# Kernel tuning notes

Measured on AMD Instinct MI355X. Metric: run time of the kernel, lower is better.

The kernel has to match this reference:

```python
import jax, jax.numpy as jnp
import numpy as np

N, E = 50000, 640000
D_IN, D_OUT, N_BASES = 128, 128, 8


def setup_inputs() -> dict:
    key = jax.random.key(0)
    k1, k2, k3, k4, k5, k6 = jax.random.split(key, 6)
    x = jax.random.normal(k1, (N, D_IN), dtype=jnp.float32)
    edge_index = jax.random.randint(k2, (2, E), 0, N, dtype=jnp.int64)
    # basis-decomposed relation weights (num_relations=1)
    bases = jax.random.normal(k3, (N_BASES, D_IN, D_OUT), dtype=jnp.float32) * 0.05
    comp = jax.random.normal(k4, (1, N_BASES), dtype=jnp.float32)
    root = jax.random.normal(k5, (D_IN, D_OUT), dtype=jnp.float32) * 0.05
    bias = jax.random.normal(k6, (D_OUT,), dtype=jnp.float32) * 0.01
    return {"x": x, "edge_index": edge_index, "bases": bases,
            "comp": comp, "root": root, "bias": bias}


def reference(x, edge_index, bases, comp, root, bias):
    # W[rel=0] = sum_b comp[0,b] * bases[b]  -> [D_IN, D_OUT]
    W = jnp.einsum('b,bio->io', comp[0], bases)
    src = edge_index[0]  # message sources (x_j)
    dst = edge_index[1]  # aggregation targets
    # gather -> scatter-add (aggr='add'), then relation-specific transform
    agg = jax.ops.segment_sum(x[src], dst, num_segments=x.shape[0])  # [N, D_IN]
    out = agg @ W + x @ root + bias  # root/self-loop transform + bias
    return out
```

## Files before the change

kernel.cpp:

```cpp
#include <hip/hip_runtime.h>

#define N_NODES 50000
#define N_EDGES 640000
#define D 128
#define NB 8
#define PAD 64
#define BM 64
#define LDA 136

typedef _Float16 half_t;
typedef __attribute__((ext_vector_type(8))) _Float16 half8;
typedef __attribute__((ext_vector_type(4))) float f32x4;

__device__ __forceinline__ void add4(float4& acc, const float4& v) {
    acc.x += v.x; acc.y += v.y; acc.z += v.z; acc.w += v.w;
}

__global__ __launch_bounds__(256)
void compute_Wt_kernel(const float* __restrict__ bases,
                       const float* __restrict__ comp,
                       const float* __restrict__ root,
                       half_t* __restrict__ Wt,
                       half_t* __restrict__ Rt) {
    int idx = blockIdx.x * 256 + threadIdx.x;
    if (idx >= D * D) return;
    int i = idx >> 7, o = idx & 127;
    float acc = 0.f;
#pragma unroll
    for (int b = 0; b < NB; ++b)
        acc += comp[b] * bases[((size_t)b * D + i) * D + o];
    Wt[o * D + i] = (half_t)acc;
    Rt[o * D + i] = (half_t)root[idx];
}

__global__ __launch_bounds__(256)
void zero_cnt_kernel(int* __restrict__ cnt) {
    int i = blockIdx.x * 256 + threadIdx.x;
    if (i < N_NODES) cnt[i] = 0;
}

__global__ __launch_bounds__(256)
void gemm_mfma_kernel(const float* __restrict__ x,
                      const half_t* __restrict__ Wt,
                      const half_t* __restrict__ Rt,
                      const float* __restrict__ bias,
                      half_t* __restrict__ y,
                      float* __restrict__ out) {
    __shared__ __align__(16) half_t As[BM * LDA];
    const int row0 = blockIdx.x * BM;
    const int tid  = threadIdx.x;

    {
        int r  = tid >> 2;
        int cc = (tid & 3) * 32;
        if (row0 + r < N_NODES) {
            const float4* x4 = (const float4*)x;
            size_t base = (size_t)(row0 + r) * 32 + (cc >> 2);
#pragma unroll
            for (int u = 0; u < 4; ++u) {
                float4 v0 = x4[base + 2 * u];
                float4 v1 = x4[base + 2 * u + 1];
                half8 h;
                h[0] = (half_t)v0.x; h[1] = (half_t)v0.y;
                h[2] = (half_t)v0.z; h[3] = (half_t)v0.w;
                h[4] = (half_t)v1.x; h[5] = (half_t)v1.y;
                h[6] = (half_t)v1.z; h[7] = (half_t)v1.w;
                *(half8*)&As[r * LDA + cc + u * 8] = h;
            }
        }
    }
    __syncthreads();

    const int wave = tid >> 6;
    const int lane = tid & 63;
    const int m    = lane & 15;
    const int quad = lane >> 4;

    half8 a[4];
#pragma unroll
    for (int kk = 0; kk < 4; ++kk)
        a[kk] = *(const half8*)&As[(wave * 16 + m) * LDA + kk * 32 + quad * 8];

    f32x4 accW[8], accR[8];
#pragma unroll
    for (int nt = 0; nt < 8; ++nt) {
        accW[nt] = (f32x4){0.f, 0.f, 0.f, 0.f};
        accR[nt] = (f32x4){0.f, 0.f, 0.f, 0.f};
    }

#pragma unroll
    for (int nt = 0; nt < 8; ++nt) {
        const half_t* wp = Wt + (nt * 16 + m) * D + quad * 8;
        const half_t* rp = Rt + (nt * 16 + m) * D + quad * 8;
        half8 bw[4], br[4];
#pragma unroll
        for (int kk = 0; kk < 4; ++kk) {
            bw[kk] = *(const half8*)(wp + kk * 32);
            br[kk] = *(const half8*)(rp + kk * 32);
        }
#pragma unroll
        for (int kk = 0; kk < 4; ++kk) {
            accW[nt] = __builtin_amdgcn_mfma_f32_16x16x32_f16(a[kk], bw[kk], accW[nt], 0, 0, 0);
            accR[nt] = __builtin_amdgcn_mfma_f32_16x16x32_f16(a[kk], br[kk], accR[nt], 0, 0, 0);
        }
    }

#pragma unroll
    for (int nt = 0; nt < 8; ++nt) {
        int col = nt * 16 + m;
        float bb = bias[col];
#pragma unroll
        for (int r = 0; r < 4; ++r) {
            int row = row0 + wave * 16 + quad * 4 + r;
            if (row < N_NODES) {
                y[(size_t)row * D + col]   = (half_t)accW[nt][r];
                out[(size_t)row * D + col] = accR[nt][r] + bb;
            }
        }
    }
}

__global__ __launch_bounds__(256)
void bucket_kernel(const int* __restrict__ eidx,
                   const half_t* __restrict__ y,
                   float* __restrict__ out,
                   int* __restrict__ cnt,
                   int* __restrict__ bucket) {
    int e = blockIdx.x * 256 + threadIdx.x;
    if (e >= N_EDGES) return;
    int src = eidx[e];
    int dst = eidx[N_EDGES + e];
    int pos = atomicAdd(&cnt[dst], 1);
    if (pos < PAD) {
        bucket[(size_t)dst * PAD + pos] = src;
    } else {
        const half_t* yr = y + (size_t)src * D;
        float* op = out + (size_t)dst * D;
        for (int q = 0; q < D; ++q) atomicAdd(op + q, (float)yr[q]);
    }
}

__global__ __launch_bounds__(256)
void gather_kernel(const int* __restrict__ cnt,
                   const int* __restrict__ bucket,
                   const half_t* __restrict__ y,
                   float* __restrict__ out) {
    int node = blockIdx.x * 16 + (threadIdx.x >> 4);
    int q = threadIdx.x & 15;
    if (node >= N_NODES) return;
    int c = cnt[node];
    if (c > PAD) c = PAD;
    const int* b = bucket + (size_t)node * PAD;
    float acc[8] = {0.f, 0.f, 0.f, 0.f, 0.f, 0.f, 0.f, 0.f};
    int i = 0;
    for (; i + 4 <= c; i += 4) {
        int4 s = *(const int4*)(b + i);
        half8 v0 = *(const half8*)(y + (size_t)s.x * D + q * 8);
        half8 v1 = *(const half8*)(y + (size_t)s.y * D + q * 8);
        half8 v2 = *(const half8*)(y + (size_t)s.z * D + q * 8);
        half8 v3 = *(const half8*)(y + (size_t)s.w * D + q * 8);
#pragma unroll
        for (int j = 0; j < 8; ++j)
            acc[j] += (float)v0[j] + (float)v1[j] + (float)v2[j] + (float)v3[j];
    }
    for (; i < c; ++i) {
        half8 v = *(const half8*)(y + (size_t)b[i] * D + q * 8);
#pragma unroll
        for (int j = 0; j < 8; ++j) acc[j] += (float)v[j];
    }
    float4* op = (float4*)(out + (size_t)node * D + q * 8);
    float4 o0 = op[0], o1 = op[1];
    o0.x += acc[0]; o0.y += acc[1]; o0.z += acc[2]; o0.w += acc[3];
    o1.x += acc[4]; o1.y += acc[5]; o1.z += acc[6]; o1.w += acc[7];
    op[0] = o0; op[1] = o1;
}

extern "C" void kernel_launch(void* const* d_in, const int* in_sizes, int n_in,
                              void* d_out, int out_size, void* d_ws, size_t ws_size,
                              hipStream_t stream) {
    const float* x     = (const float*)d_in[0];
    const int*   eidx  = (const int*)d_in[1];
    const float* bases = (const float*)d_in[2];
    const float* comp  = (const float*)d_in[3];
    const float* root  = (const float*)d_in[4];
    const float* bias  = (const float*)d_in[5];
    float* out = (float*)d_out;

    char* ws = (char*)d_ws;
    half_t* y      = (half_t*)ws;
    half_t* Wt     = (half_t*)(ws + 12800000);
    half_t* Rt     = (half_t*)(ws + 12832768);
    int*    cnt    = (int*)(ws + 12865536);
    int*    bucket = (int*)(ws + 13065536);

    zero_cnt_kernel<<<(N_NODES + 255) / 256, 256, 0, stream>>>(cnt);
    compute_Wt_kernel<<<(D * D + 255) / 256, 256, 0, stream>>>(bases, comp, root, Wt, Rt);
    gemm_mfma_kernel<<<(N_NODES + BM - 1) / BM, 256, 0, stream>>>(x, Wt, Rt, bias, y, out);
    bucket_kernel<<<(N_EDGES + 255) / 256, 256, 0, stream>>>(eidx, y, out, cnt, bucket);
    gather_kernel<<<(N_NODES + 15) / 16, 256, 0, stream>>>(cnt, bucket, y, out);
}
```

Before: 183.5 us.

## Fuse init kernels, load GEMM A-fragments directly, shrink bucket pad, unroll gather

Merges the counter-zeroing and weight-composition kernels into one launch. The GEMM now loads and converts x straight into MFMA A-fragments in registers instead of staging through shared memory with a barrier. The per-node bucket pad drops from 64 to 32, which shrinks bucket memory but sends more overflow edges down the slow per-element atomic path. The gather loop is unrolled to 8 neighbours to keep more loads in flight.

```diff
diff --git a/kernel.cpp b/kernel.cpp
--- a/kernel.cpp
+++ b/kernel.cpp
@@ -4,82 +4,65 @@
 #define N_EDGES 640000
 #define D 128
 #define NB 8
-#define PAD 64
+#define PAD 32
 #define BM 64
-#define LDA 136
 
 typedef _Float16 half_t;
 typedef __attribute__((ext_vector_type(8))) _Float16 half8;
 typedef __attribute__((ext_vector_type(4))) float f32x4;
 
-__device__ __forceinline__ void add4(float4& acc, const float4& v) {
-    acc.x += v.x; acc.y += v.y; acc.z += v.z; acc.w += v.w;
-}
-
-__global__ __launch_bounds__(256)
-void compute_Wt_kernel(const float* __restrict__ bases,
-                       const float* __restrict__ comp,
-                       const float* __restrict__ root,
-                       half_t* __restrict__ Wt,
-                       half_t* __restrict__ Rt) {
-    int idx = blockIdx.x * 256 + threadIdx.x;
-    if (idx >= D * D) return;
-    int i = idx >> 7, o = idx & 127;
-    float acc = 0.f;
-#pragma unroll
-    for (int b = 0; b < NB; ++b)
-        acc += comp[b] * bases[((size_t)b * D + i) * D + o];
-    Wt[o * D + i] = (half_t)acc;
-    Rt[o * D + i] = (half_t)root[idx];
-}
-
-__global__ __launch_bounds__(256)
-void zero_cnt_kernel(int* __restrict__ cnt) {
+__global__ __launch_bounds__(256)
+void init_kernel(const float* __restrict__ bases,
+                 const float* __restrict__ comp,
+                 const float* __restrict__ root,
+                 half_t* __restrict__ Wt,
+                 half_t* __restrict__ Rt,
+                 int* __restrict__ cnt) {
     int i = blockIdx.x * 256 + threadIdx.x;
     if (i < N_NODES) cnt[i] = 0;
-}
-
-__global__ __launch_bounds__(256)
-void gemm_mfma_kernel(const float* __restrict__ x,
-                      const half_t* __restrict__ Wt,
-                      const half_t* __restrict__ Rt,
-                      const float* __restrict__ bias,
-                      half_t* __restrict__ y,
-                      float* __restrict__ out) {
-    __shared__ __align__(16) half_t As[BM * LDA];
-    const int row0 = blockIdx.x * BM;
+    if (i < D * D) {
+        int ii = i >> 7, o = i & 127;
+        float acc = 0.f;
+#pragma unroll
+        for (int b = 0; b < NB; ++b)
+            acc += comp[b] * bases[((size_t)b * D + ii) * D + o];
+        Wt[o * D + ii] = (half_t)acc;
+        Rt[o * D + ii] = (half_t)root[i];
+    }
+}
+
+__global__ __launch_bounds__(256)
+void gemm_kernel(const float* __restrict__ x,
+                 const half_t* __restrict__ Wt,
+                 const half_t* __restrict__ Rt,
+                 const float* __restrict__ bias,
+                 half_t* __restrict__ y,
+                 float* __restrict__ out) {
     const int tid  = threadIdx.x;
-
-    {
-        int r  = tid >> 2;
-        int cc = (tid & 3) * 32;
-        if (row0 + r < N_NODES) {
-            const float4* x4 = (const float4*)x;
-            size_t base = (size_t)(row0 + r) * 32 + (cc >> 2);
-#pragma unroll
-            for (int u = 0; u < 4; ++u) {
-                float4 v0 = x4[base + 2 * u];
-                float4 v1 = x4[base + 2 * u + 1];
-                half8 h;
-                h[0] = (half_t)v0.x; h[1] = (half_t)v0.y;
-                h[2] = (half_t)v0.z; h[3] = (half_t)v0.w;
-                h[4] = (half_t)v1.x; h[5] = (half_t)v1.y;
-                h[6] = (half_t)v1.z; h[7] = (half_t)v1.w;
-                *(half8*)&As[r * LDA + cc + u * 8] = h;
-            }
-        }
-    }
-    __syncthreads();
-
     const int wave = tid >> 6;
     const int lane = tid & 63;
     const int m    = lane & 15;
     const int quad = lane >> 4;
-
+    const int row0 = blockIdx.x * BM;
+    const int arow = row0 + wave * 16 + m;
+
+    const float4* x4 = (const float4*)x;
+    size_t abase = (size_t)(arow < N_NODES ? arow : 0) * 32 + quad * 2;
+    float4 xa[8];
+#pragma unroll
+    for (int kk = 0; kk < 4; ++kk) {
+        xa[2 * kk]     = x4[abase + kk * 8];
+        xa[2 * kk + 1] = x4[abase + kk * 8 + 1];
+    }
     half8 a[4];
 #pragma unroll
-    for (int kk = 0; kk < 4; ++kk)
-        a[kk] = *(const half8*)&As[(wave * 16 + m) * LDA + kk * 32 + quad * 8];
+    for (int kk = 0; kk < 4; ++kk) {
+        float4 v0 = xa[2 * kk], v1 = xa[2 * kk + 1];
+        half8 h;
+        h[0] = (half_t)v0.x; h[1] = (half_t)v0.y; h[2] = (half_t)v0.z; h[3] = (half_t)v0.w;
+        h[4] = (half_t)v1.x; h[5] = (half_t)v1.y; h[6] = (half_t)v1.z; h[7] = (half_t)v1.w;
+        a[kk] = h;
+    }
 
     f32x4 accW[8], accR[8];
 #pragma unroll
@@ -87,7 +70,6 @@
         accW[nt] = (f32x4){0.f, 0.f, 0.f, 0.f};
         accR[nt] = (f32x4){0.f, 0.f, 0.f, 0.f};
     }
-
 #pragma unroll
     for (int nt = 0; nt < 8; ++nt) {
         const half_t* wp = Wt + (nt * 16 + m) * D + quad * 8;
@@ -104,7 +86,6 @@
             accR[nt] = __builtin_amdgcn_mfma_f32_16x16x32_f16(a[kk], br[kk], accR[nt], 0, 0, 0);
         }
     }
-
 #pragma unroll
     for (int nt = 0; nt < 8; ++nt) {
         int col = nt * 16 + m;
@@ -153,6 +134,22 @@
     const int* b = bucket + (size_t)node * PAD;
     float acc[8] = {0.f, 0.f, 0.f, 0.f, 0.f, 0.f, 0.f, 0.f};
     int i = 0;
+    for (; i + 8 <= c; i += 8) {
+        int4 s0 = *(const int4*)(b + i);
+        int4 s1 = *(const int4*)(b + i + 4);
+        half8 v0 = *(const half8*)(y + (size_t)s0.x * D + q * 8);
+        half8 v1 = *(const half8*)(y + (size_t)s0.y * D + q * 8);
+        half8 v2 = *(const half8*)(y + (size_t)s0.z * D + q * 8);
+        half8 v3 = *(const half8*)(y + (size_t)s0.w * D + q * 8);
+        half8 v4 = *(const half8*)(y + (size_t)s1.x * D + q * 8);
+        half8 v5 = *(const half8*)(y + (size_t)s1.y * D + q * 8);
+        half8 v6 = *(const half8*)(y + (size_t)s1.z * D + q * 8);
+        half8 v7 = *(const half8*)(y + (size_t)s1.w * D + q * 8);
+#pragma unroll
+        for (int j = 0; j < 8; ++j)
+            acc[j] += ((float)v0[j] + (float)v1[j]) + ((float)v2[j] + (float)v3[j])
+                    + ((float)v4[j] + (float)v5[j]) + ((float)v6[j] + (float)v7[j]);
+    }
     for (; i + 4 <= c; i += 4) {
         int4 s = *(const int4*)(b + i);
         half8 v0 = *(const half8*)(y + (size_t)s.x * D + q * 8);
@@ -161,7 +158,7 @@
         half8 v3 = *(const half8*)(y + (size_t)s.w * D + q * 8);
 #pragma unroll
         for (int j = 0; j < 8; ++j)
-            acc[j] += (float)v0[j] + (float)v1[j] + (float)v2[j] + (float)v3[j];
+            acc[j] += ((float)v0[j] + (float)v1[j]) + ((float)v2[j] + (float)v3[j]);
     }
     for (; i < c; ++i) {
         half8 v = *(const half8*)(y + (size_t)b[i] * D + q * 8);
@@ -190,12 +187,15 @@
     half_t* y      = (half_t*)ws;
     half_t* Wt     = (half_t*)(ws + 12800000);
     half_t* Rt     = (half_t*)(ws + 12832768);
-    int*    cnt    = (int*)(ws + 12865536);
-    int*    bucket = (int*)(ws + 13065536);
-
-    zero_cnt_kernel<<<(N_NODES + 255) / 256, 256, 0, stream>>>(cnt);
-    compute_Wt_kernel<<<(D * D + 255) / 256, 256, 0, stream>>>(bases, comp, root, Wt, Rt);
-    gemm_mfma_kernel<<<(N_NODES + BM - 1) / BM, 256, 0, stream>>>(x, Wt, Rt, bias, y, out);
-    bucket_kernel<<<(N_EDGES + 255) / 256, 256, 0, stream>>>(eidx, y, out, cnt, bucket);
-    gather_kernel<<<(N_NODES + 15) / 16, 256, 0, stream>>>(cnt, bucket, y, out);
-}
+    int*    cnt    = (int*)   (ws + 12865536);
+    int*    bucket = (int*)   (ws + 13065536);
+
+    init_kernel<<<(N_NODES + 255) / 256, 256, 0, stream>>>(
+        bases, comp, root, Wt, Rt, cnt);
+    gemm_kernel<<<(N_NODES + BM - 1) / BM, 256, 0, stream>>>(
+        x, Wt, Rt, bias, y, out);
+    bucket_kernel<<<(N_EDGES + 255) / 256, 256, 0, stream>>>(
+        eidx, y, out, cnt, bucket);
+    gather_kernel<<<(N_NODES + 15) / 16, 256, 0, stream>>>(
+        cnt, bucket, y, out);
+}
```

After: 181.9 us. Within noise of the previous version (-0.8%).
